# Performance work log

Hardware: AMD Instinct MI355X
Metric: run time of the kernel (lower is better)

## Reference

```python
import jax, jax.numpy as jnp
import numpy as np

ITEM_NUM = 100000
EMBED = 128
HIDDEN = 256
BETA = 0.5
B = 4096
H = 200

def setup_inputs() -> dict:
    key = jax.random.key(0)
    ks = jax.random.split(key, 7)
    history = jax.random.randint(ks[0], (B, H), 0, ITEM_NUM)
    target = jax.random.randint(ks[1], (B,), 0, ITEM_NUM)
    embed_history = jax.random.normal(ks[2], (ITEM_NUM, EMBED), dtype=jnp.float32) * 0.01
    embed_target = jax.random.normal(ks[3], (ITEM_NUM, EMBED), dtype=jnp.float32) * 0.01
    # nn.Linear default init: U(-1/sqrt(fan_in), 1/sqrt(fan_in)); biases zeroed by _init_weight_
    lim1 = 1.0 / np.sqrt(EMBED)
    W1 = jax.random.uniform(ks[4], (EMBED, HIDDEN), dtype=jnp.float32, minval=-lim1, maxval=lim1)
    b1 = jnp.zeros((HIDDEN,), dtype=jnp.float32)
    lim2 = 1.0 / np.sqrt(HIDDEN)
    w2 = jax.random.uniform(ks[5], (HIDDEN,), dtype=jnp.float32, minval=-lim2, maxval=lim2)
    return {"history": history, "target": target, "embed_history": embed_history,
            "embed_target": embed_target, "W1": W1, "b1": b1, "w2": w2}

def reference(history, target, embed_history, embed_target, W1, b1, w2):
    hist_e = embed_history[history]            # [B, H, d]
    tgt_e = embed_target[target][:, None, :]   # [B, 1, d]
    x = hist_e * tgt_e                          # [B, H, d]
    a = jnp.einsum('bhk,k->bh', jax.nn.relu(jnp.einsum('bhd,dk->bhk', x, W1) + b1), w2)  # [B, H]
    mask = (history != target[:, None]).astype(a.dtype)  # [B, H]
    exp_A = jnp.exp(a) * mask                  # [B, H]
    denom = jnp.sum(exp_A, axis=-1) ** BETA    # [B], beta-power normalization (not softmax)
    attn = exp_A / denom[:, None]              # [B, H]
    pred = jnp.einsum('bh,bhd,bd->b', attn, hist_e, tgt_e[:, 0, :])  # [B]
    return jax.nn.sigmoid(pred)
```

## Files before the change

### kernel.cpp

```cpp
#include <hip/hip_runtime.h>

#define B_SZ   4096
#define H_SZ   200
#define D_SZ   128
#define N_SZ   256
#define ROWS   (B_SZ * H_SZ)
#define BM     64
#define TPB    8
#define RPB    (BM * TPB)
#define NBLK   (ROWS / RPB)

typedef __attribute__((ext_vector_type(8))) short bf16x8;
typedef __attribute__((ext_vector_type(2))) float f32x2;
typedef __attribute__((ext_vector_type(4))) float f32x4;

__device__ __forceinline__ unsigned short f2bf(float f) {
    unsigned u = __builtin_bit_cast(unsigned, f);
    u += 0x7FFFu + ((u >> 16) & 1u);
    return (unsigned short)(u >> 16);
}
__device__ __forceinline__ unsigned bfpack(f32x2 x) {
    return __builtin_amdgcn_perm(__builtin_bit_cast(unsigned, x[1]),
                                 __builtin_bit_cast(unsigned, x[0]), 0x07060302u);
}

__global__ __launch_bounds__(256) void cvt_w1(const float* __restrict__ src,
                                              unsigned short* __restrict__ dst) {
    int i = blockIdx.x * 256 + threadIdx.x;
    int n = i >> 7, d = i & 127;
    dst[i] = f2bf(src[d * N_SZ + n]);
}

__global__ __launch_bounds__(512, 4) void nais_main(
    const int* __restrict__ history, const int* __restrict__ target,
    const float* __restrict__ eh, const float* __restrict__ et,
    const unsigned short* __restrict__ w1t, const float* __restrict__ b1,
    const float* __restrict__ w2,
    float* __restrict__ a_out, float* __restrict__ dotd_out)
{
    __shared__ uint4 AbufV[2][BM * 256 / 16];
    __shared__ float apart[2][8][BM];
    __shared__ float tgt_f[4][D_SZ];
    __shared__ int   tgt_i[4];

    const int tid  = threadIdx.x;
    const int wid  = tid >> 6;
    const int lane = tid & 63;
    const int lo   = lane & 15;
    const int hi   = lane >> 4;
    const int row  = tid >> 3;
    const int seg  = tid & 7;
    const int blk  = blockIdx.x;
    const int b_base = (blk * RPB) / H_SZ;

    if (tid < 4) {
        int bb = b_base + tid;
        tgt_i[tid] = target[bb < B_SZ ? bb : (B_SZ - 1)];
    }
    __syncthreads();
    {
        const int r4 = tid >> 7, d = tid & 127;
        tgt_f[r4][d] = et[(size_t)tgt_i[r4] * D_SZ + d];
    }

    bf16x8 wfrag[4][2];
    #pragma unroll
    for (int ni = 0; ni < 2; ++ni) {
        int n = 32 * wid + 16 * ni + lo;
        #pragma unroll
        for (int ki = 0; ki < 4; ++ki)
            wfrag[ki][ni] = *(const bf16x8*)(w1t + (size_t)n * D_SZ + 32 * ki + 8 * hi);
    }
    const int n0 = 32 * wid + 4 * hi;
    const f32x4 b1a = *(const f32x4*)(b1 + n0);
    const f32x4 b1b = *(const f32x4*)(b1 + n0 + 16);
    const f32x4 w2a = *(const f32x4*)(w2 + n0);
    const f32x4 w2b = *(const f32x4*)(w2 + n0 + 16);

    const int grow0 = blk * RPB + row;
    const int* hrow = history + grow0;
    int ih_cur = hrow[0];
    int ih_nxt = hrow[BM];
    f32x4 hq0, hq1, hq2, hq3;
    {
        const f32x4* p = (const f32x4*)(eh + (size_t)ih_cur * D_SZ + 16 * seg);
        hq0 = p[0]; hq1 = p[1]; hq2 = p[2]; hq3 = p[3];
    }
    int b_loc = grow0 / H_SZ - b_base;
    int rem   = grow0 - (b_loc + b_base) * H_SZ;
    __syncthreads();

    for (int t = 0; t < TPB; ++t) {
        char* Ab = (char*)AbufV[t & 1];
        const int gr = grow0 + t * BM;

        {
            const f32x2* tp = (const f32x2*)&tgt_f[b_loc][16 * seg];
            f32x2 h[8];
            h[0] = f32x2{hq0[0], hq0[1]}; h[1] = f32x2{hq0[2], hq0[3]};
            h[2] = f32x2{hq1[0], hq1[1]}; h[3] = f32x2{hq1[2], hq1[3]};
            h[4] = f32x2{hq2[0], hq2[1]}; h[5] = f32x2{hq2[2], hq2[3]};
            h[6] = f32x2{hq3[0], hq3[1]}; h[7] = f32x2{hq3[2], hq3[3]};
            f32x2 x[8];
            #pragma unroll
            for (int j = 0; j < 8; ++j) x[j] = h[j] * tp[j];
            f32x2 acc01 = x[0] + x[1], acc23 = x[2] + x[3];
            f32x2 acc45 = x[4] + x[5], acc67 = x[6] + x[7];
            f32x2 accA = acc01 + acc23, accB = acc45 + acc67;
            f32x2 accT = accA + accB;
            float s = accT[0] + accT[1];
            s += __shfl_xor(s, 1);
            s += __shfl_xor(s, 2);
            s += __shfl_xor(s, 4);
            if (seg == 0) dotd_out[gr] = s;
            uint4 o1 = uint4{bfpack(x[0]), bfpack(x[1]), bfpack(x[2]), bfpack(x[3])};
            uint4 o2 = uint4{bfpack(x[4]), bfpack(x[5]), bfpack(x[6]), bfpack(x[7])};
            const unsigned sw = (unsigned)((row & 7) << 4);
            char* rb = Ab + row * 256;
            *(uint4*)(rb + (((unsigned)(32 * seg)) ^ sw))      = o1;
            *(uint4*)(rb + (((unsigned)(32 * seg + 16)) ^ sw)) = o2;
        }
        __syncthreads();

        if (t + 1 < TPB) {
            ih_cur = ih_nxt;
            if (t + 2 < TPB) ih_nxt = hrow[(t + 2) * BM];
            const f32x4* p = (const f32x4*)(eh + (size_t)ih_cur * D_SZ + 16 * seg);
            hq0 = p[0]; hq1 = p[1]; hq2 = p[2]; hq3 = p[3];
        }

        if (t > 0 && tid < BM) {
            const float* ap = &apart[(t - 1) & 1][0][tid];
            float a = ap[0];
            #pragma unroll
            for (int w = 1; w < 8; ++w) a += ap[w * BM];
            a_out[blk * RPB + (t - 1) * BM + tid] = a;
        }

        #pragma unroll
        for (int mi = 0; mi < 4; ++mi) {
            const int rr = 16 * mi + lo;
            const unsigned swr = (unsigned)((rr & 7) << 4);
            bf16x8 af[4];
            #pragma unroll
            for (int ki = 0; ki < 4; ++ki) {
                unsigned off = ((unsigned)(64 * ki + 16 * hi)) ^ swr;
                af[ki] = *(const bf16x8*)(Ab + rr * 256 + off);
            }
            f32x4 acc0 = b1a;
            f32x4 acc1 = b1b;
            __builtin_amdgcn_s_setprio(1);
            #pragma unroll
            for (int ki = 0; ki < 4; ++ki) {
                acc0 = __builtin_amdgcn_mfma_f32_16x16x32_bf16(wfrag[ki][0], af[ki], acc0, 0, 0, 0);
                acc1 = __builtin_amdgcn_mfma_f32_16x16x32_bf16(wfrag[ki][1], af[ki], acc1, 0, 0, 0);
            }
            __builtin_amdgcn_s_setprio(0);
            float v = fmaxf(acc0[0], 0.f) * w2a[0] + fmaxf(acc1[0], 0.f) * w2b[0];
            v += fmaxf(acc0[1], 0.f) * w2a[1] + fmaxf(acc1[1], 0.f) * w2b[1];
            v += fmaxf(acc0[2], 0.f) * w2a[2] + fmaxf(acc1[2], 0.f) * w2b[2];
            v += fmaxf(acc0[3], 0.f) * w2a[3] + fmaxf(acc1[3], 0.f) * w2b[3];
            v += __shfl_xor(v, 16);
            v += __shfl_xor(v, 32);
            if (lane < 16) apart[t & 1][wid][16 * mi + lane] = v;
        }

        rem += BM;
        if (rem >= H_SZ) { rem -= H_SZ; ++b_loc; }
    }
    __syncthreads();
    if (tid < BM) {
        const float* ap = &apart[(TPB - 1) & 1][0][tid];
        float a = ap[0];
        #pragma unroll
        for (int w = 1; w < 8; ++w) a += ap[w * BM];
        a_out[blk * RPB + (TPB - 1) * BM + tid] = a;
    }
}

__global__ __launch_bounds__(64) void nais_finish(
    const int* __restrict__ history, const int* __restrict__ target,
    const float* __restrict__ a_in, const float* __restrict__ dotd_in,
    float* __restrict__ out)
{
    const int b    = blockIdx.x;
    const int lane = threadIdx.x;
    const int tgt  = target[b];
    float s1 = 0.f, s2 = 0.f;
    for (int h = lane; h < H_SZ; h += 64) {
        int rg = b * H_SZ + h;
        float e = (history[rg] != tgt) ? __expf(a_in[rg]) : 0.f;
        s1 += e;
        s2 += e * dotd_in[rg];
    }
    #pragma unroll
    for (int o = 1; o < 64; o <<= 1) {
        s1 += __shfl_xor(s1, o);
        s2 += __shfl_xor(s2, o);
    }
    if (lane == 0) {
        float pred = s2 / sqrtf(s1);
        out[b] = 1.f / (1.f + __expf(-pred));
    }
}

extern "C" void kernel_launch(void* const* d_in, const int* in_sizes, int n_in,
                              void* d_out, int out_size, void* d_ws, size_t ws_size,
                              hipStream_t stream) {
    const int*   history = (const int*)d_in[0];
    const int*   target  = (const int*)d_in[1];
    const float* eh      = (const float*)d_in[2];
    const float* et      = (const float*)d_in[3];
    const float* W1      = (const float*)d_in[4];
    const float* b1      = (const float*)d_in[5];
    const float* w2      = (const float*)d_in[6];
    float* out = (float*)d_out;

    char* ws = (char*)d_ws;
    unsigned short* w1t = (unsigned short*)ws;
    float* a_ws    = (float*)(ws + N_SZ * D_SZ * 2);
    float* dotd_ws = a_ws + ROWS;

    cvt_w1<<<(N_SZ * D_SZ) / 256, 256, 0, stream>>>(W1, w1t);
    nais_main<<<NBLK, 512, 0, stream>>>(history, target, eh, et, w1t, b1, w2, a_ws, dotd_ws);
    nais_finish<<<B_SZ, 64, 0, stream>>>(history, target, a_ws, dotd_ws, out);
}
```

Measured before the change: 96.87 us.

## Halve tiles per block and split row gathers into two contiguous halves

Cuts tiles per block from 8 to 4, which doubles the grid size and gives more blocks for latency hiding and load balance. Each thread now loads 8 contiguous floats from each half of the embedding row instead of 16 contiguous floats, so a wavefront's gather touches two 128-byte spans per row and coalesces better. The LDS write pattern changes so the bf16 operand layout seen by the MFMA reads stays the same. More blocks also means more per-block setup: weight-fragment loads and target fetches are repeated twice as often.

```diff
diff --git a/kernel.cpp b/kernel.cpp
--- a/kernel.cpp
+++ b/kernel.cpp
@@ -6,12 +6,11 @@
 #define N_SZ   256
 #define ROWS   (B_SZ * H_SZ)
 #define BM     64
-#define TPB    8
+#define TPB    4
 #define RPB    (BM * TPB)
 #define NBLK   (ROWS / RPB)
 
 typedef __attribute__((ext_vector_type(8))) short bf16x8;
-typedef __attribute__((ext_vector_type(2))) float f32x2;
 typedef __attribute__((ext_vector_type(4))) float f32x4;
 
 __device__ __forceinline__ unsigned short f2bf(float f) {
@@ -19,9 +18,9 @@
     u += 0x7FFFu + ((u >> 16) & 1u);
     return (unsigned short)(u >> 16);
 }
-__device__ __forceinline__ unsigned bfpack(f32x2 x) {
-    return __builtin_amdgcn_perm(__builtin_bit_cast(unsigned, x[1]),
-                                 __builtin_bit_cast(unsigned, x[0]), 0x07060302u);
+__device__ __forceinline__ unsigned bfpack2(float a, float b) {
+    return __builtin_amdgcn_perm(__builtin_bit_cast(unsigned, b),
+                                 __builtin_bit_cast(unsigned, a), 0x07060302u);
 }
 
 __global__ __launch_bounds__(256) void cvt_w1(const float* __restrict__ src,
@@ -83,8 +82,9 @@
     int ih_nxt = hrow[BM];
     f32x4 hq0, hq1, hq2, hq3;
     {
-        const f32x4* p = (const f32x4*)(eh + (size_t)ih_cur * D_SZ + 16 * seg);
-        hq0 = p[0]; hq1 = p[1]; hq2 = p[2]; hq3 = p[3];
+        const float* base = eh + (size_t)ih_cur * D_SZ + 8 * seg;
+        hq0 = *(const f32x4*)(base);      hq1 = *(const f32x4*)(base + 4);
+        hq2 = *(const f32x4*)(base + 64); hq3 = *(const f32x4*)(base + 68);
     }
     int b_loc = grow0 / H_SZ - b_base;
     int rem   = grow0 - (b_loc + b_base) * H_SZ;
@@ -95,38 +95,33 @@
         const int gr = grow0 + t * BM;
 
         {
-            const f32x2* tp = (const f32x2*)&tgt_f[b_loc][16 * seg];
-            f32x2 h[8];
-            h[0] = f32x2{hq0[0], hq0[1]}; h[1] = f32x2{hq0[2], hq0[3]};
-            h[2] = f32x2{hq1[0], hq1[1]}; h[3] = f32x2{hq1[2], hq1[3]};
-            h[4] = f32x2{hq2[0], hq2[1]}; h[5] = f32x2{hq2[2], hq2[3]};
-            h[6] = f32x2{hq3[0], hq3[1]}; h[7] = f32x2{hq3[2], hq3[3]};
-            f32x2 x[8];
-            #pragma unroll
-            for (int j = 0; j < 8; ++j) x[j] = h[j] * tp[j];
-            f32x2 acc01 = x[0] + x[1], acc23 = x[2] + x[3];
-            f32x2 acc45 = x[4] + x[5], acc67 = x[6] + x[7];
-            f32x2 accA = acc01 + acc23, accB = acc45 + acc67;
-            f32x2 accT = accA + accB;
-            float s = accT[0] + accT[1];
+            const float* tp = &tgt_f[b_loc][8 * seg];
+            f32x4 t0 = *(const f32x4*)(tp);      f32x4 t1 = *(const f32x4*)(tp + 4);
+            f32x4 t2 = *(const f32x4*)(tp + 64); f32x4 t3 = *(const f32x4*)(tp + 68);
+            f32x4 x0 = hq0 * t0, x1 = hq1 * t1, x2 = hq2 * t2, x3 = hq3 * t3;
+            f32x4 sx = (x0 + x1) + (x2 + x3);
+            float s = (sx[0] + sx[1]) + (sx[2] + sx[3]);
             s += __shfl_xor(s, 1);
             s += __shfl_xor(s, 2);
             s += __shfl_xor(s, 4);
             if (seg == 0) dotd_out[gr] = s;
-            uint4 o1 = uint4{bfpack(x[0]), bfpack(x[1]), bfpack(x[2]), bfpack(x[3])};
-            uint4 o2 = uint4{bfpack(x[4]), bfpack(x[5]), bfpack(x[6]), bfpack(x[7])};
+            uint4 o1 = uint4{bfpack2(x0[0], x0[1]), bfpack2(x0[2], x0[3]),
+                             bfpack2(x1[0], x1[1]), bfpack2(x1[2], x1[3])};
+            uint4 o2 = uint4{bfpack2(x2[0], x2[1]), bfpack2(x2[2], x2[3]),
+                             bfpack2(x3[0], x3[1]), bfpack2(x3[2], x3[3])};
             const unsigned sw = (unsigned)((row & 7) << 4);
             char* rb = Ab + row * 256;
-            *(uint4*)(rb + (((unsigned)(32 * seg)) ^ sw))      = o1;
-            *(uint4*)(rb + (((unsigned)(32 * seg + 16)) ^ sw)) = o2;
+            *(uint4*)(rb + (((unsigned)(16 * seg)) ^ sw))          = o1;
+            *(uint4*)(rb + (128u + (((unsigned)(16 * seg)) ^ sw))) = o2;
         }
         __syncthreads();
 
         if (t + 1 < TPB) {
             ih_cur = ih_nxt;
             if (t + 2 < TPB) ih_nxt = hrow[(t + 2) * BM];
-            const f32x4* p = (const f32x4*)(eh + (size_t)ih_cur * D_SZ + 16 * seg);
-            hq0 = p[0]; hq1 = p[1]; hq2 = p[2]; hq3 = p[3];
+            const float* base = eh + (size_t)ih_cur * D_SZ + 8 * seg;
+            hq0 = *(const f32x4*)(base);      hq1 = *(const f32x4*)(base + 4);
+            hq2 = *(const f32x4*)(base + 64); hq3 = *(const f32x4*)(base + 68);
         }
 
         if (t > 0 && tid < BM) {
```

Measured after the change: 94.09 us. 2.9% less time.
